# Optimization experiments

Hardware: AMD Instinct MI355X
Metric: run time of the kernel (lower is better)

The kernel has to match this reference:

```python
import jax, jax.numpy as jnp
import numpy as np

DIM = 512          # model dim
DH = 32            # dim_head
WSZ = 8            # window_size
HEADS = DIM // DH  # 16
INNER = HEADS * DH # 512
D4 = DIM // 4      # DPB hidden = 128
EPS = 1e-5


def _ln(x, g, b=None, eps=EPS):
    m = jnp.mean(x, axis=-1, keepdims=True)
    v = jnp.var(x, axis=-1, keepdims=True)
    y = (x - m) * jax.lax.rsqrt(v + eps) * g
    return y if b is None else y + b


def setup_inputs() -> dict:
    key = jax.random.key(0)
    ks = jax.random.split(key, 8)
    g = lambda k, shape, s=0.02: (jax.random.normal(k, shape, jnp.float32) * s)
    return {
        "x": jax.random.normal(ks[0], (16, 64, 64, DIM), jnp.float32),
        "norm_g": jnp.ones((DIM,), jnp.float32),
        "norm_b": jnp.zeros((DIM,), jnp.float32),
        "w_qkv": g(ks[1], (DIM, 3 * INNER)),
        "w_out": g(ks[2], (INNER, DIM)),
        "b_out": jnp.zeros((DIM,), jnp.float32),
        "dpb_w0": g(ks[3], (2, D4)), "dpb_b0": jnp.zeros((D4,), jnp.float32), "dpb_ln0": jnp.ones((D4,), jnp.float32),
        "dpb_w1": g(ks[4], (D4, D4)), "dpb_b1": jnp.zeros((D4,), jnp.float32), "dpb_ln1": jnp.ones((D4,), jnp.float32),
        "dpb_w2": g(ks[5], (D4, D4)), "dpb_b2": jnp.zeros((D4,), jnp.float32), "dpb_ln2": jnp.ones((D4,), jnp.float32),
        "dpb_w3": g(ks[6], (D4, 1)), "dpb_b3": jnp.zeros((1,), jnp.float32),
    }


def reference(x, norm_g, norm_b, w_qkv, w_out, b_out,
              dpb_w0, dpb_b0, dpb_ln0,
              dpb_w1, dpb_b1, dpb_ln1,
              dpb_w2, dpb_b2, dpb_ln2,
              dpb_w3, dpb_b3):
    B, H, W, d = x.shape
    w = WSZ
    scale = DH ** -0.5

    x = _ln(x, norm_g, norm_b)

    # 'short' attention: partition into non-overlapping wxw windows
    # b (h s1) (w s2) d -> (b h w) s1 s2 d
    xw = x.reshape(B, H // w, w, W // w, w, d).transpose(0, 1, 3, 2, 4, 5)
    xw = xw.reshape(-1, w, w, d)  # [nb, w, w, d]

    qkv = xw @ w_qkv  # 1x1 conv == dense, no bias
    q, k, v = jnp.split(qkv, 3, axis=-1)
    to_heads = lambda t: t.reshape(t.shape[0], w * w, HEADS, DH).transpose(0, 2, 1, 3)
    q, k, v = map(to_heads, (q, k, v))  # [nb, h, w*w, dh]

    sim = jnp.einsum('bhid,bhjd->bhij', q * scale, k)  # [nb, h, w*w, w*w]

    # relative-position gather indices (static)
    pos = jnp.arange(w)
    grid = jnp.stack(jnp.meshgrid(pos, pos, indexing='ij'), axis=-1).reshape(-1, 2)
    rel = grid[:, None] - grid[None, :] + (w - 1)
    rel_pos_indices = rel[..., 0] * (2 * w - 1) + rel[..., 1]  # [w*w, w*w]

    # dynamic position bias MLP over the (2w+1)^2 relative offsets
    p = jnp.arange(-w, w + 1)
    rp = jnp.stack(jnp.meshgrid(p, p, indexing='ij'), axis=-1).reshape(-1, 2).astype(jnp.float32)
    h = jax.nn.relu(_ln(rp @ dpb_w0 + dpb_b0, dpb_ln0))
    h = jax.nn.relu(_ln(h @ dpb_w1 + dpb_b1, dpb_ln1))
    h = jax.nn.relu(_ln(h @ dpb_w2 + dpb_b2, dpb_ln2))
    biases = (h @ dpb_w3 + dpb_b3)[:, 0]  # [(2w+1)^2]

    sim = sim + biases[rel_pos_indices]
    attn = jax.nn.softmax(sim, axis=-1)
    out = jnp.einsum('bhij,bhjd->bhid', attn, v)

    out = out.transpose(0, 2, 1, 3).reshape(-1, w, w, INNER)
    out = out @ w_out + b_out  # 1x1 conv with bias

    # (b h w) s1 s2 d -> b (h s1) (w s2) d
    out = out.reshape(B, H // w, W // w, w, w, d).transpose(0, 1, 3, 2, 4, 5)
    return out.reshape(B, H, W, d)
```

## Files before the change

### kernel.cpp

```cpp
#include <hip/hip_runtime.h>
#include <cstdint>
#include <cstddef>

typedef unsigned short u16;
typedef __attribute__((ext_vector_type(8))) short short8;
typedef __attribute__((ext_vector_type(4))) float f32x4;
typedef __attribute__((ext_vector_type(4))) unsigned short us4;

#define AS1 __attribute__((address_space(1)))
#define AS3 __attribute__((address_space(3)))

__device__ __forceinline__ u16 f2bf(float f) {
  union { float f; unsigned u; } v; v.f = f;
  unsigned r = v.u + 0x7fffu + ((v.u >> 16) & 1u);
  return (u16)(r >> 16);
}

__device__ __forceinline__ void gload_lds16(const u16* g, u16* l) {
  __builtin_amdgcn_global_load_lds((AS1 void*)g, (AS3 void*)l, 16, 0, 0);
}

__global__ void ln_cast_kernel(const float* __restrict__ x, const float* __restrict__ g,
                               const float* __restrict__ b, u16* __restrict__ out) {
  const int lane = threadIdx.x & 63;
  const int tok = blockIdx.x * 4 + (threadIdx.x >> 6);
  const float4* row = (const float4*)(x + (size_t)tok * 512);
  float4 v0 = row[lane];
  float4 v1 = row[lane + 64];
  float s = v0.x + v0.y + v0.z + v0.w + v1.x + v1.y + v1.z + v1.w;
  float q = v0.x*v0.x + v0.y*v0.y + v0.z*v0.z + v0.w*v0.w
          + v1.x*v1.x + v1.y*v1.y + v1.z*v1.z + v1.w*v1.w;
#pragma unroll
  for (int m = 1; m < 64; m <<= 1) { s += __shfl_xor(s, m, 64); q += __shfl_xor(q, m, 64); }
  const float mean = s * (1.0f / 512.0f);
  const float var = q * (1.0f / 512.0f) - mean * mean;
  const float r = rsqrtf(var + 1e-5f);
  const float4* g4 = (const float4*)g;
  const float4* b4 = (const float4*)b;
  float4 ga = g4[lane], gb = g4[lane + 64];
  float4 ba = b4[lane], bb = b4[lane + 64];
  us4 o0 = { f2bf((v0.x - mean) * r * ga.x + ba.x), f2bf((v0.y - mean) * r * ga.y + ba.y),
             f2bf((v0.z - mean) * r * ga.z + ba.z), f2bf((v0.w - mean) * r * ga.w + ba.w) };
  us4 o1 = { f2bf((v1.x - mean) * r * gb.x + bb.x), f2bf((v1.y - mean) * r * gb.y + bb.y),
             f2bf((v1.z - mean) * r * gb.z + bb.z), f2bf((v1.w - mean) * r * gb.w + bb.w) };
  *(us4*)(out + (size_t)tok * 512 + lane * 4) = o0;
  *(us4*)(out + (size_t)tok * 512 + 256 + lane * 4) = o1;
}

__global__ void prep_w_kernel(const float* __restrict__ wqkv, const float* __restrict__ wout,
                              u16* __restrict__ wqkvT, u16* __restrict__ woutT) {
  int idx = blockIdx.x * blockDim.x + threadIdx.x;
  if (idx < 512 * 1536) {
    int n = idx >> 9, k = idx & 511;
    wqkvT[idx] = f2bf(wqkv[k * 1536 + n]);
  } else {
    int j = idx - 512 * 1536;
    if (j < 512 * 512) {
      int n = j >> 9, k = j & 511;
      woutT[j] = f2bf(wout[k * 512 + n]);
    }
  }
}

__device__ __forceinline__ float lnrelu128(float a, float g, float* red, int tid) {
  float s = a, q = a * a;
#pragma unroll
  for (int m = 1; m < 64; m <<= 1) { s += __shfl_xor(s, m, 64); q += __shfl_xor(q, m, 64); }
  __syncthreads();
  if ((tid & 63) == 0) { red[tid >> 6] = s; red[2 + (tid >> 6)] = q; }
  __syncthreads();
  float S = red[0] + red[1], Q = red[2] + red[3];
  float mean = S * (1.f / 128.f);
  float var = Q * (1.f / 128.f) - mean * mean;
  float y = (a - mean) * rsqrtf(var + 1e-5f) * g;
  return fmaxf(y, 0.f);
}

__global__ void dpb_mlp_kernel(const float* __restrict__ w0, const float* __restrict__ b0, const float* __restrict__ g0,
                               const float* __restrict__ w1, const float* __restrict__ b1, const float* __restrict__ g1,
                               const float* __restrict__ w2, const float* __restrict__ b2, const float* __restrict__ g2,
                               const float* __restrict__ w3, const float* __restrict__ b3,
                               float* __restrict__ biases) {
  __shared__ float h[128];
  __shared__ float red[4];
  const int tid = threadIdx.x;
  const int row = blockIdx.x;
  const float p0 = (float)(row / 17) - 8.0f;
  const float p1 = (float)(row % 17) - 8.0f;
  float a = p0 * w0[tid] + p1 * w0[128 + tid] + b0[tid];
  a = lnrelu128(a, g0[tid], red, tid);
  h[tid] = a;
  __syncthreads();
  float acc = b1[tid];
  for (int i = 0; i < 128; ++i) acc += h[i] * w1[i * 128 + tid];
  acc = lnrelu128(acc, g1[tid], red, tid);
  h[tid] = acc;
  __syncthreads();
  float acc2 = b2[tid];
  for (int i = 0; i < 128; ++i) acc2 += h[i] * w2[i * 128 + tid];
  acc2 = lnrelu128(acc2, g2[tid], red, tid);
  float t = acc2 * w3[tid];
#pragma unroll
  for (int m = 1; m < 64; m <<= 1) t += __shfl_xor(t, m, 64);
  __syncthreads();
  if ((tid & 63) == 0) red[tid >> 6] = t;
  __syncthreads();
  if (tid == 0) biases[row] = red[0] + red[1] + b3[0];
}

__global__ void dpb_table_kernel(const float* __restrict__ biases, float* __restrict__ table) {
  int t = blockIdx.x * blockDim.x + threadIdx.x;
  if (t < 4096) {
    int i = t >> 6, j = t & 63;
    int r0 = (i >> 3) - (j >> 3) + 7;
    int r1 = (i & 7) - (j & 7) + 7;
    table[t] = biases[r0 * 15 + r1];
  }
}

template <int CT, bool F32OUT>
__global__ __launch_bounds__(256, 4) void gemm_bk64_kernel(const u16* __restrict__ A, const u16* __restrict__ BT,
                                                           void* __restrict__ Cv, const float* __restrict__ bias) {
  __shared__ __align__(16) u16 As[128 * 64];
  __shared__ __align__(16) u16 Bs[128 * 64];
  const int tid = threadIdx.x;
  const int w = tid >> 6, l = tid & 63;
  const int wr = w >> 1, wc = w & 1;
  const int cr = l & 15, cg = l >> 4;
  const int hcr = (cr + ((cr >> 3) << 2)) & 7;

  const int hw = blockIdx.x;
  const int ix = hw >> 3;
  const int rt = (hw & 7) + 8 * (ix / CT);
  const int ct = ix % CT;
  const size_t brow = (size_t)rt * 128;
  const size_t bcol = (size_t)ct * 128;
  const int N = CT * 128;

  const int srow8 = tid >> 3;
  const int hsrc = ((srow8 & 15) + (((srow8 >> 3) & 1) << 2)) & 7;
  const int csrc = ((tid & 7) ^ hsrc) * 8;
  const u16* gA = A + (brow + srow8) * 512 + csrc;
  const u16* gB = BT + (bcol + srow8) * 512 + csrc;

  const f32x4 zero = {0.f, 0.f, 0.f, 0.f};
  f32x4 acc[4][4];
#pragma unroll
  for (int i = 0; i < 4; ++i)
#pragma unroll
    for (int j = 0; j < 4; ++j) acc[i][j] = zero;

  const u16* aP = &As[(wr * 64 + cr) * 64];
  const u16* bP = &Bs[(wc * 64 + cr) * 64];

  for (int k0 = 0; k0 < 512; k0 += 64) {
#pragma unroll
    for (int j = 0; j < 4; ++j) {
      gload_lds16(gA + (size_t)j * 32 * 512 + k0, &As[j * 2048 + w * 512]);
      gload_lds16(gB + (size_t)j * 32 * 512 + k0, &Bs[j * 2048 + w * 512]);
    }
    __syncthreads();
#pragma unroll
    for (int ks = 0; ks < 2; ++ks) {
      short8 af[4], bf[4];
      const int pco = ((ks * 4 + cg) ^ hcr) * 8;
#pragma unroll
      for (int fr = 0; fr < 4; ++fr) af[fr] = *(const short8*)(aP + fr * 1024 + pco);
#pragma unroll
      for (int fc = 0; fc < 4; ++fc) bf[fc] = *(const short8*)(bP + fc * 1024 + pco);
#pragma unroll
      for (int fr = 0; fr < 4; ++fr)
#pragma unroll
        for (int fc = 0; fc < 4; ++fc)
          acc[fr][fc] = __builtin_amdgcn_mfma_f32_16x16x32_bf16(bf[fc], af[fr], acc[fr][fc], 0, 0, 0);
    }
    __syncthreads();
  }

  if (F32OUT) {
    float* C = (float*)Cv;
#pragma unroll
    for (int fc = 0; fc < 4; ++fc) {
      size_t col = bcol + wc * 64 + fc * 16 + cg * 4;
      float4 bv = *(const float4*)&bias[col];
#pragma unroll
      for (int fr = 0; fr < 4; ++fr) {
        size_t r = brow + wr * 64 + fr * 16 + cr;
        float4 o = { acc[fr][fc][0] + bv.x, acc[fr][fc][1] + bv.y,
                     acc[fr][fc][2] + bv.z, acc[fr][fc][3] + bv.w };
        *(float4*)(C + r * N + col) = o;
      }
    }
  } else {
    u16* C = (u16*)Cv;
#pragma unroll
    for (int fc = 0; fc < 4; ++fc) {
      size_t col = bcol + wc * 64 + fc * 16 + cg * 4;
#pragma unroll
      for (int fr = 0; fr < 4; ++fr) {
        size_t r = brow + wr * 64 + fr * 16 + cr;
        uint2 p;
        p.x = (unsigned)f2bf(acc[fr][fc][0]) | ((unsigned)f2bf(acc[fr][fc][1]) << 16);
        p.y = (unsigned)f2bf(acc[fr][fc][2]) | ((unsigned)f2bf(acc[fr][fc][3]) << 16);
        *(uint2*)(C + r * N + col) = p;
      }
    }
  }
}

__global__ __launch_bounds__(256, 4) void attn_kernel(const u16* __restrict__ qkv,
                                                      const float* __restrict__ table,
                                                      u16* __restrict__ aout) {
  __shared__ __align__(16) u16 VT[4][32 * 74];
  const int l = threadIdx.x & 63;
  const int wv = threadIdx.x >> 6;
  const int pair = blockIdx.x * 4 + wv;
  const int head = pair & 15;
  const int win = pair >> 4;
  const int base = ((win >> 6) << 12) + (((win >> 3) & 7) << 9) + ((win & 7) << 3);
  const int cr = l & 15, cg = l >> 4;
  u16* vt = VT[wv];

  short8 qf[4], kf[4];
  {
    short8 vl[4];
#pragma unroll
    for (int i = 0; i < 4; ++i) {
      int t = i * 16 + cr;
      size_t row = base + ((t >> 3) << 6) + (t & 7);
      const u16* rp = qkv + row * 1536 + head * 32 + cg * 8;
      qf[i] = *(const short8*)(rp);
      kf[i] = *(const short8*)(rp + 512);
      vl[i] = *(const short8*)(rp + 1024);
    }
#pragma unroll
    for (int mt = 0; mt < 4; ++mt)
#pragma unroll
      for (int j = 0; j < 8; ++j)
        vt[(cg * 8 + j) * 74 + mt * 16 + cr] = (u16)vl[mt][j];
  }

  asm volatile("s_waitcnt lgkmcnt(0)" ::: "memory");
  __builtin_amdgcn_sched_barrier(0);
  short8 vfT[2][2];
#pragma unroll
  for (int dt = 0; dt < 2; ++dt)
#pragma unroll
    for (int kk = 0; kk < 2; ++kk)
      vfT[dt][kk] = *(const short8*)&vt[(dt * 16 + cr) * 74 + kk * 32 + cg * 8];

  const f32x4 zero = {0.f, 0.f, 0.f, 0.f};
  const float scale = 0.17677669529663689f;
  const int laneA = cr + 32 * (cg & 1);
  const int hi = cg >> 1;

#pragma unroll
  for (int nt = 0; nt < 4; ++nt) {
    f32x4 s4[4];
    __builtin_amdgcn_s_setprio(1);
#pragma unroll
    for (int mt = 0; mt < 4; ++mt)
      s4[mt] = __builtin_amdgcn_mfma_f32_16x16x32_bf16(kf[mt], qf[nt], zero, 0, 0, 0);
    __builtin_amdgcn_s_setprio(0);

    float p[16];
    float mx = -3.0e38f;
#pragma unroll
    for (int mt = 0; mt < 4; ++mt) {
      float4 tb = *(const float4*)&table[(nt * 16 + cr) * 64 + mt * 16 + cg * 4];
      p[mt * 4 + 0] = s4[mt][0] * scale + tb.x;
      p[mt * 4 + 1] = s4[mt][1] * scale + tb.y;
      p[mt * 4 + 2] = s4[mt][2] * scale + tb.z;
      p[mt * 4 + 3] = s4[mt][3] * scale + tb.w;
      mx = fmaxf(mx, fmaxf(fmaxf(p[mt * 4], p[mt * 4 + 1]), fmaxf(p[mt * 4 + 2], p[mt * 4 + 3])));
    }
    mx = fmaxf(mx, __shfl_xor(mx, 16, 64));
    mx = fmaxf(mx, __shfl_xor(mx, 32, 64));
    float sum = 0.f;
#pragma unroll
    for (int i = 0; i < 16; ++i) { p[i] = __expf(p[i] - mx); sum += p[i]; }
    sum += __shfl_xor(sum, 16, 64);
    sum += __shfl_xor(sum, 32, 64);
    const float inv = 1.0f / sum;

    unsigned pk[4][2];
#pragma unroll
    for (int mt = 0; mt < 4; ++mt)
#pragma unroll
      for (int i = 0; i < 2; ++i)
        pk[mt][i] = (unsigned)f2bf(p[mt * 4 + 2 * i] * inv) | ((unsigned)f2bf(p[mt * 4 + 2 * i + 1] * inv) << 16);

    f32x4 o2[2] = {zero, zero};
#pragma unroll
    for (int kk = 0; kk < 2; ++kk) {
      union { unsigned u[4]; short8 v; } pf;
#pragma unroll
      for (int i = 0; i < 2; ++i) {
        unsigned x0 = (unsigned)__shfl((int)pk[2 * kk][i], laneA, 64);
        unsigned x1 = (unsigned)__shfl((int)pk[2 * kk + 1][i], laneA, 64);
        unsigned y0 = (unsigned)__shfl((int)pk[2 * kk][i], laneA + 16, 64);
        unsigned y1 = (unsigned)__shfl((int)pk[2 * kk + 1][i], laneA + 16, 64);
        pf.u[i] = hi ? x1 : x0;
        pf.u[2 + i] = hi ? y1 : y0;
      }
      __builtin_amdgcn_s_setprio(1);
#pragma unroll
      for (int dt = 0; dt < 2; ++dt)
        o2[dt] = __builtin_amdgcn_mfma_f32_16x16x32_bf16(vfT[dt][kk], pf.v, o2[dt], 0, 0, 0);
      __builtin_amdgcn_s_setprio(0);
    }

    int t = nt * 16 + cr;
    size_t row = base + ((t >> 3) << 6) + (t & 7);
#pragma unroll
    for (int dt = 0; dt < 2; ++dt) {
      uint2 pck;
      pck.x = (unsigned)f2bf(o2[dt][0]) | ((unsigned)f2bf(o2[dt][1]) << 16);
      pck.y = (unsigned)f2bf(o2[dt][2]) | ((unsigned)f2bf(o2[dt][3]) << 16);
      *(uint2*)(aout + row * 512 + head * 32 + dt * 16 + cg * 4) = pck;
    }
  }
}

extern "C" void kernel_launch(void* const* d_in, const int* in_sizes, int n_in,
                              void* d_out, int out_size, void* d_ws, size_t ws_size,
                              hipStream_t stream) {
  const float* x = (const float*)d_in[0];
  const float* norm_g = (const float*)d_in[1];
  const float* norm_b = (const float*)d_in[2];
  const float* w_qkv = (const float*)d_in[3];
  const float* w_out = (const float*)d_in[4];
  const float* b_out = (const float*)d_in[5];
  const float* dw0 = (const float*)d_in[6];
  const float* db0 = (const float*)d_in[7];
  const float* dg0 = (const float*)d_in[8];
  const float* dw1 = (const float*)d_in[9];
  const float* db1 = (const float*)d_in[10];
  const float* dg1 = (const float*)d_in[11];
  const float* dw2 = (const float*)d_in[12];
  const float* db2 = (const float*)d_in[13];
  const float* dg2 = (const float*)d_in[14];
  const float* dw3 = (const float*)d_in[15];
  const float* db3 = (const float*)d_in[16];

  char* ws = (char*)d_ws;
  size_t off = 0;
  auto take = [&](size_t bytes) { char* p = ws + off; off += (bytes + 255) & ~(size_t)255; return p; };
  u16* xln = (u16*)take(65536ull * 512 * 2);
  u16* wqkvT = (u16*)take(1536 * 512 * 2);
  u16* woutT = (u16*)take(512 * 512 * 2);
  float* biases = (float*)take(289 * 4);
  float* table = (float*)take(4096 * 4);

  ln_cast_kernel<<<16384, 256, 0, stream>>>(x, norm_g, norm_b, xln);
  prep_w_kernel<<<4096, 256, 0, stream>>>(w_qkv, w_out, wqkvT, woutT);
  dpb_mlp_kernel<<<289, 128, 0, stream>>>(dw0, db0, dg0, dw1, db1, dg1, dw2, db2, dg2, dw3, db3, biases);
  dpb_table_kernel<<<16, 256, 0, stream>>>(biases, table);

  size_t rem = (ws_size > off) ? ws_size - off : 0;
  int nch = 4;
  if (rem >= 32768ull * 2048 * 2 + 512) nch = 2;
  const int rows = 65536 / nch;
  u16* qkvbuf = (u16*)take((size_t)rows * 1536 * 2);
  u16* attnbuf = (u16*)take((size_t)rows * 512 * 2);

  for (int c = 0; c < nch; ++c) {
    const u16* Ac = xln + (size_t)c * rows * 512;
    gemm_bk64_kernel<12, false><<<(rows / 128) * 12, 256, 0, stream>>>(Ac, wqkvT, (void*)qkvbuf, nullptr);
    attn_kernel<<<(rows / 64) * 16 / 4, 256, 0, stream>>>(qkvbuf, table, attnbuf);
    float* Cc = (float*)d_out + (size_t)c * rows * 512;
    gemm_bk64_kernel<4, true><<<(rows / 128) * 4, 256, 0, stream>>>(attnbuf, woutT, (void*)Cc, b_out);
  }
}
```

Before: 334.1 us.

## Fuse window attention with output projection in one kernel per window

Each 1024-thread block now handles one 8x8 window with all 16 heads, one per wave. The attention output is written to a swizzled LDS tile instead of global memory, and the output projection GEMM (plus bias) is then done from LDS, with each wave computing 32 output columns. This removes the attnbuf round trip and the separate output GEMM launch. In exchange, every block rereads the full 512x512 woutT from global/L2, and the large LDS footprint and 1024-thread blocks limit occupancy.

```diff
diff --git a/kernel.cpp b/kernel.cpp
--- a/kernel.cpp
+++ b/kernel.cpp
@@ -208,18 +208,18 @@
   }
 }
 
-__global__ __launch_bounds__(256, 4) void attn_kernel(const u16* __restrict__ qkv,
-                                                      const float* __restrict__ table,
-                                                      u16* __restrict__ aout) {
-  __shared__ __align__(16) u16 VT[4][32 * 74];
+__global__ __launch_bounds__(1024, 4) void attn_out_kernel(const u16* __restrict__ qkv,
+                                                           const float* __restrict__ table,
+                                                           const u16* __restrict__ woutT,
+                                                           const float* __restrict__ bias,
+                                                           float* __restrict__ Cout) {
+  __shared__ __align__(16) u16 lds[37888];
   const int l = threadIdx.x & 63;
   const int wv = threadIdx.x >> 6;
-  const int pair = blockIdx.x * 4 + wv;
-  const int head = pair & 15;
-  const int win = pair >> 4;
+  const int win = blockIdx.x;
   const int base = ((win >> 6) << 12) + (((win >> 3) & 7) << 9) + ((win & 7) << 3);
   const int cr = l & 15, cg = l >> 4;
-  u16* vt = VT[wv];
+  u16* vt = &lds[wv * 2368];
 
   short8 qf[4], kf[4];
   {
@@ -228,7 +228,7 @@
     for (int i = 0; i < 4; ++i) {
       int t = i * 16 + cr;
       size_t row = base + ((t >> 3) << 6) + (t & 7);
-      const u16* rp = qkv + row * 1536 + head * 32 + cg * 8;
+      const u16* rp = qkv + row * 1536 + wv * 32 + cg * 8;
       qf[i] = *(const short8*)(rp);
       kf[i] = *(const short8*)(rp + 512);
       vl[i] = *(const short8*)(rp + 1024);
@@ -239,7 +239,6 @@
       for (int j = 0; j < 8; ++j)
         vt[(cg * 8 + j) * 74 + mt * 16 + cr] = (u16)vl[mt][j];
   }
-
   asm volatile("s_waitcnt lgkmcnt(0)" ::: "memory");
   __builtin_amdgcn_sched_barrier(0);
   short8 vfT[2][2];
@@ -248,11 +247,15 @@
 #pragma unroll
     for (int kk = 0; kk < 2; ++kk)
       vfT[dt][kk] = *(const short8*)&vt[(dt * 16 + cr) * 74 + kk * 32 + cg * 8];
+  asm volatile("s_waitcnt lgkmcnt(0)" ::: "memory");
+  __builtin_amdgcn_sched_barrier(0);
+  __syncthreads();
 
   const f32x4 zero = {0.f, 0.f, 0.f, 0.f};
   const float scale = 0.17677669529663689f;
   const int laneA = cr + 32 * (cg & 1);
   const int hi = cg >> 1;
+  const int e2 = 2 * (cr & 7);
 
 #pragma unroll
   for (int nt = 0; nt < 4; ++nt) {
@@ -310,14 +313,48 @@
       __builtin_amdgcn_s_setprio(0);
     }
 
-    int t = nt * 16 + cr;
-    size_t row = base + ((t >> 3) << 6) + (t & 7);
+    const int t = nt * 16 + cr;
 #pragma unroll
     for (int dt = 0; dt < 2; ++dt) {
       uint2 pck;
       pck.x = (unsigned)f2bf(o2[dt][0]) | ((unsigned)f2bf(o2[dt][1]) << 16);
       pck.y = (unsigned)f2bf(o2[dt][2]) | ((unsigned)f2bf(o2[dt][3]) << 16);
-      *(uint2*)(aout + row * 512 + head * 32 + dt * 16 + cg * 4) = pck;
+      const int c4 = wv * 8 + dt * 4 + cg;
+      *(uint2*)&lds[t * 512 + (c4 ^ e2) * 4] = pck;
+    }
+  }
+  __syncthreads();
+
+  f32x4 acc[4][2];
+#pragma unroll
+  for (int fr = 0; fr < 4; ++fr) { acc[fr][0] = zero; acc[fr][1] = zero; }
+#pragma unroll
+  for (int ks = 0; ks < 16; ++ks) {
+    short8 af[4], bf[2];
+#pragma unroll
+    for (int fr = 0; fr < 4; ++fr)
+      af[fr] = *(const short8*)&lds[(fr * 16 + cr) * 512 + (((ks * 8 + cg * 2) ^ e2) << 2)];
+#pragma unroll
+    for (int fc = 0; fc < 2; ++fc)
+      bf[fc] = *(const short8*)&woutT[(size_t)(wv * 32 + fc * 16 + cr) * 512 + ks * 32 + cg * 8];
+#pragma unroll
+    for (int fr = 0; fr < 4; ++fr)
+#pragma unroll
+      for (int fc = 0; fc < 2; ++fc)
+        acc[fr][fc] = __builtin_amdgcn_mfma_f32_16x16x32_bf16(bf[fc], af[fr], acc[fr][fc], 0, 0, 0);
+  }
+
+#pragma unroll
+  for (int fc = 0; fc < 2; ++fc) {
+    const int col = wv * 32 + fc * 16 + cg * 4;
+    float4 bv = *(const float4*)&bias[col];
+#pragma unroll
+    for (int fr = 0; fr < 4; ++fr) {
+      const int tr = fr * 16 + cr;
+      size_t g = base + ((tr >> 3) << 6) + (tr & 7);
+      float4 o = { acc[fr][fc][0] + bv.x, acc[fr][fc][1] + bv.y,
+                   acc[fr][fc][2] + bv.z, acc[fr][fc][3] + bv.w };
+      *(float4*)(Cout + g * 512 + col) = o;
     }
   }
 }
@@ -359,16 +396,14 @@
 
   size_t rem = (ws_size > off) ? ws_size - off : 0;
   int nch = 4;
-  if (rem >= 32768ull * 2048 * 2 + 512) nch = 2;
+  if (rem >= 32768ull * 1536 * 2 + 512) nch = 2;
   const int rows = 65536 / nch;
   u16* qkvbuf = (u16*)take((size_t)rows * 1536 * 2);
-  u16* attnbuf = (u16*)take((size_t)rows * 512 * 2);
 
   for (int c = 0; c < nch; ++c) {
     const u16* Ac = xln + (size_t)c * rows * 512;
     gemm_bk64_kernel<12, false><<<(rows / 128) * 12, 256, 0, stream>>>(Ac, wqkvT, (void*)qkvbuf, nullptr);
-    attn_kernel<<<(rows / 64) * 16 / 4, 256, 0, stream>>>(qkvbuf, table, attnbuf);
     float* Cc = (float*)d_out + (size_t)c * rows * 512;
-    gemm_bk64_kernel<4, true><<<(rows / 128) * 4, 256, 0, stream>>>(attnbuf, woutT, (void*)Cc, b_out);
-  }
-}
+    attn_out_kernel<<<rows / 64, 1024, 0, stream>>>(qkvbuf, table, woutT, b_out, Cc);
+  }
+}
```

Measured after the change: 358.6 us. 1.07x slower.
